# Optimization experiments

Hardware: AMD Instinct MI355X
Metric: run time of the kernel (lower is better)

## Reference

```python
import jax, jax.numpy as jnp
import numpy as np


def c2p_gather(feat, ind):
    # feat: [B, C, M] cell features; ind: [B, N, 2] (slot 0 = cell index)
    B, C, _ = feat.shape
    idx = ind[:, :, 0]                                   # [B, N]
    idx3 = jnp.broadcast_to(idx[:, None, :], (B, C, idx.shape[1]))
    return jnp.take_along_axis(feat, idx3, axis=2)       # [B, C, N]


def p2c_scatter(x, ind, num_cells):
    # x: [B, C, Nn] point features; ind: [B, Nn, 2]; scatter-add into [B, C, M]
    idx = ind[:, :, 0]                                   # [B, Nn]

    def per_batch(xb, ib):
        # xb: [C, Nn] -> segment_sum over points -> [M, C]
        return jax.ops.segment_sum(xb.T, ib, num_segments=num_cells).T

    return jax.vmap(per_batch)(x, idx)                   # [B, C, M]


def setup_inputs() -> dict:
    key = jax.random.key(0)
    ks = jax.random.split(key, 8)
    B, Cv, Cr, E, Co = 2, 64, 20, 64, 64
    Mv, Mr = 100000, 50000
    N = 262144            # gathered points; os=8 -> bundle=4 -> Nn=65536 nodes
    Nn = N // 4
    return {
        "v_feat": jax.random.normal(ks[0], (B, Cv, Mv), jnp.float32),
        "r_feat": jax.random.normal(ks[1], (B, Cr, Mr), jnp.float32),
        "Wq": jax.random.normal(ks[2], (E, Cr), jnp.float32) * 0.1,
        "Wk": jax.random.normal(ks[3], (E, Cv), jnp.float32) * 0.1,
        "Wv": jax.random.normal(ks[4], (E, Cv), jnp.float32) * 0.1,
        "Wo": jax.random.normal(ks[5], (Co, E), jnp.float32) * 0.1,
        "v2p_ind": jax.random.randint(ks[6], (B, N, 2), 0, Mv).astype(jnp.int64),
        "r2p_ind": jax.random.randint(ks[7], (B, Nn, 2), 0, Mr).astype(jnp.int64),
        "os": 8,
    }


def reference(v_feat, r_feat, Wq, Wk, Wv, Wo, v2p_ind, r2p_ind, os):
    bundle = max(1, int(os) // 2)
    B, Cv, _ = v_feat.shape
    Mr = r_feat.shape[2]

    # c2p gather of detached features (module calls .detach())
    v_pp = c2p_gather(jax.lax.stop_gradient(v_feat), v2p_ind)       # [B, Cv, N]
    N = v_pp.shape[2]
    Nn = N // bundle
    v_nodes = v_pp.reshape(B, Cv, Nn, bundle)                        # bundle splits
    r_pp = c2p_gather(jax.lax.stop_gradient(r_feat), r2p_ind)        # [B, Cr, Nn]

    # attent1d: query from r feature, keys/values from the neighbor bundle
    E = Wq.shape[0]
    q = jnp.einsum("ec,bcn->ben", Wq, r_pp)                          # [B, E, Nn]
    k = jnp.einsum("ec,bcnm->benm", Wk, v_nodes)                     # [B, E, Nn, bundle]
    v = jnp.einsum("ec,bcnm->benm", Wv, v_nodes)
    scores = jnp.einsum("ben,benm->bnm", q, k) / jnp.sqrt(jnp.float32(E))
    attn = jax.nn.softmax(scores, axis=-1)                           # over bundle
    agg = jnp.einsum("bnm,benm->ben", attn, v)                       # [B, E, Nn]
    xr = jnp.einsum("oe,ben->bon", Wo, agg)                          # [B, Co, Nn]

    # p2c scatter back to r-cell layout (size taken from r_feat)
    xr_mapped = p2c_scatter(xr, r2p_ind, Mr)                         # [B, Co, Mr]
    return xr_mapped
```

## Files before the change

### kernel.cpp

```cpp
#include <hip/hip_runtime.h>
#include <cstdint>

#define BB 2
#define CV 64
#define CR 20
#define EE 64
#define CO 64

__global__ __launch_bounds__(256) void k_prep(
    const float* __restrict__ Wq, const float* __restrict__ Wk,
    const float* __restrict__ Wv, const float* __restrict__ Wo,
    const int* __restrict__ r2p, float* __restrict__ G,
    float* __restrict__ H, int* __restrict__ flag) {
  int bid = blockIdx.x, t = threadIdx.x;
  if (bid < 5) {
    int idx = bid * 256 + t;
    if (idx < CR * CV) {
      int cr = idx / CV, cv = idx % CV;
      float s = 0.f;
      #pragma unroll
      for (int e = 0; e < EE; ++e) s += Wq[e * CR + cr] * Wk[e * CV + cv];
      G[idx] = s;
    }
  } else if (bid < 21) {
    int idx = (bid - 5) * 256 + t;
    int o = idx >> 6, c = idx & 63;
    float s = 0.f;
    #pragma unroll
    for (int e = 0; e < EE; ++e) s += Wo[o * EE + e] * Wv[e * CV + c];
    H[idx] = s;
  } else {
    __shared__ int any;
    if (t == 0) any = 0;
    __syncthreads();
    int nz = 0;
    for (int i = t; i < 4096; i += 256) nz |= r2p[2 * i + 1];
    if (nz) atomicOr(&any, 1);
    __syncthreads();
    if (t == 0) *flag = (any == 0) ? 4 : 2;
  }
}

__global__ __launch_bounds__(256) void k_transpose_v(
    const float* __restrict__ vf, float* __restrict__ vt, int Mv, int ntm) {
  __shared__ float tile[64][65];
  int b = blockIdx.x / ntm, tm = blockIdx.x % ntm;
  int m0 = tm * 64;
  int t = threadIdx.x;
  const float* src = vf + (size_t)b * CV * Mv;
  bool fast = ((Mv & 3) == 0) && (m0 + 64 <= Mv);
  if (fast) {
    #pragma unroll
    for (int k = 0; k < 4; ++k) {
      int c = k * 16 + (t >> 4), l16 = t & 15;
      float4 v = *(const float4*)&src[(size_t)c * Mv + m0 + 4 * l16];
      tile[c][4 * l16 + 0] = v.x;
      tile[c][4 * l16 + 1] = v.y;
      tile[c][4 * l16 + 2] = v.z;
      tile[c][4 * l16 + 3] = v.w;
    }
  } else {
    #pragma unroll
    for (int k = 0; k < 16; ++k) {
      int idx = t + k * 256;
      int c = idx >> 6, ml = idx & 63;
      int m = m0 + ml;
      tile[c][ml] = (m < Mv) ? src[(size_t)c * Mv + m] : 0.f;
    }
  }
  __syncthreads();
  float* dst = vt + (size_t)b * Mv * 64;
  if (fast) {
    #pragma unroll
    for (int k = 0; k < 4; ++k) {
      int ml = k * 16 + (t >> 4), l16 = t & 15;
      float4 w;
      w.x = tile[4 * l16 + 0][ml];
      w.y = tile[4 * l16 + 1][ml];
      w.z = tile[4 * l16 + 2][ml];
      w.w = tile[4 * l16 + 3][ml];
      *(float4*)&dst[(size_t)(m0 + ml) * 64 + 4 * l16] = w;
    }
  } else {
    #pragma unroll
    for (int k = 0; k < 16; ++k) {
      int idx = t + k * 256;
      int ml = idx >> 6, c = idx & 63;
      int m = m0 + ml;
      if (m < Mv) dst[(size_t)m * 64 + c] = tile[c][ml];
    }
  }
}

__global__ __launch_bounds__(256) void k_gq(
    const float* __restrict__ rf, const float* __restrict__ G,
    float* __restrict__ gq, int Mr, int ntj) {
  __shared__ float Gl[CR * 64];
  __shared__ float rt[CR][68];
  int b = blockIdx.x / ntj, tj = blockIdx.x % ntj;
  int j0 = tj * 64;
  int t = threadIdx.x;
  for (int idx = t; idx < CR * 64; idx += 256) Gl[idx] = G[idx];
  const float* src = rf + (size_t)b * CR * Mr;
  for (int idx = t; idx < CR * 64; idx += 256) {
    int c = idx >> 6, jl = idx & 63;
    int j = j0 + jl;
    rt[c][jl] = (j < Mr) ? src[(size_t)c * Mr + j] : 0.f;
  }
  __syncthreads();
  int ti = t & 15, tjq = t >> 4;
  float acc[4][4];
  #pragma unroll
  for (int a = 0; a < 4; ++a)
    #pragma unroll
    for (int q = 0; q < 4; ++q) acc[a][q] = 0.f;
  for (int c = 0; c < CR; ++c) {
    float4 gx = *(const float4*)&Gl[c * 64 + 4 * ti];
    float4 xj = *(const float4*)&rt[c][4 * tjq];
    #pragma unroll
    for (int a = 0; a < 4; ++a) {
      float xv = (a == 0) ? xj.x : (a == 1) ? xj.y : (a == 2) ? xj.z : xj.w;
      acc[a][0] += xv * gx.x;
      acc[a][1] += xv * gx.y;
      acc[a][2] += xv * gx.z;
      acc[a][3] += xv * gx.w;
    }
  }
  #pragma unroll
  for (int a = 0; a < 4; ++a) {
    int j = j0 + 4 * tjq + a;
    if (j < Mr) {
      float4 w = make_float4(acc[a][0], acc[a][1], acc[a][2], acc[a][3]);
      *(float4*)&gq[((size_t)b * Mr + j) * 64 + 4 * ti] = w;
    }
  }
}

template <int WS>
__device__ __forceinline__ void main_loop(
    const float* __restrict__ vt, const float* __restrict__ gq,
    const int* __restrict__ v2p, const int* __restrict__ r2p,
    float* __restrict__ xs, int Mv, int Mr, int N, int Nn, int P,
    int gw, int totWaves) {
  int stride = totWaves * 2;
  int base = gw * 2;
  if (base >= P) return;
  int b = (base >= Nn) ? 1 : 0;
  int n0 = base - b * Nn;
  int j0 = r2p[((size_t)b * Nn + n0) * WS];
  int j1 = r2p[((size_t)b * Nn + n0 + 1) * WS];
  const int* vi = v2p + ((size_t)b * N + (size_t)n0 * 4) * WS;
  int i00 = vi[0 * WS], i01 = vi[1 * WS], i02 = vi[2 * WS], i03 = vi[3 * WS];
  int i10 = vi[4 * WS], i11 = vi[5 * WS], i12 = vi[6 * WS], i13 = vi[7 * WS];
  int lane = threadIdx.x & 63;
  while (base < P) {
    const float* gqb = gq + (size_t)b * Mr * 64;
    const float* vb = vt + (size_t)b * Mv * 64;
    float q0 = gqb[(size_t)j0 * 64 + lane];
    float q1 = gqb[(size_t)j1 * 64 + lane];
    float c00 = vb[(size_t)i00 * 64 + lane];
    float c01 = vb[(size_t)i01 * 64 + lane];
    float c02 = vb[(size_t)i02 * 64 + lane];
    float c03 = vb[(size_t)i03 * 64 + lane];
    float c10 = vb[(size_t)i10 * 64 + lane];
    float c11 = vb[(size_t)i11 * 64 + lane];
    float c12 = vb[(size_t)i12 * 64 + lane];
    float c13 = vb[(size_t)i13 * 64 + lane];
    size_t sj0 = ((size_t)b * Mr + j0) * 64 + lane;
    size_t sj1 = ((size_t)b * Mr + j1) * 64 + lane;
    int nb = base + stride;
    int b2 = 0, pj0 = 0, pj1 = 0;
    int p00 = 0, p01 = 0, p02 = 0, p03 = 0, p10 = 0, p11 = 0, p12 = 0, p13 = 0;
    if (nb < P) {
      b2 = (nb >= Nn) ? 1 : 0;
      int n2 = nb - b2 * Nn;
      pj0 = r2p[((size_t)b2 * Nn + n2) * WS];
      pj1 = r2p[((size_t)b2 * Nn + n2 + 1) * WS];
      const int* vi2 = v2p + ((size_t)b2 * N + (size_t)n2 * 4) * WS;
      p00 = vi2[0 * WS]; p01 = vi2[1 * WS]; p02 = vi2[2 * WS]; p03 = vi2[3 * WS];
      p10 = vi2[4 * WS]; p11 = vi2[5 * WS]; p12 = vi2[6 * WS]; p13 = vi2[7 * WS];
    }
    float s00 = q0 * c00, s01 = q0 * c01, s02 = q0 * c02, s03 = q0 * c03;
    float s10 = q1 * c10, s11 = q1 * c11, s12 = q1 * c12, s13 = q1 * c13;
    #pragma unroll
    for (int off = 32; off > 0; off >>= 1) {
      s00 += __shfl_xor(s00, off); s01 += __shfl_xor(s01, off);
      s02 += __shfl_xor(s02, off); s03 += __shfl_xor(s03, off);
      s10 += __shfl_xor(s10, off); s11 += __shfl_xor(s11, off);
      s12 += __shfl_xor(s12, off); s13 += __shfl_xor(s13, off);
    }
    {
      float a = s00 * 0.125f, b3 = s01 * 0.125f, c3 = s02 * 0.125f, d = s03 * 0.125f;
      float mx = fmaxf(fmaxf(a, b3), fmaxf(c3, d));
      float e0 = __expf(a - mx), e1 = __expf(b3 - mx);
      float e2 = __expf(c3 - mx), e3 = __expf(d - mx);
      float inv = 1.f / (e0 + e1 + e2 + e3);
      float ag = (e0 * c00 + e1 * c01 + e2 * c02 + e3 * c03) * inv;
      atomicAdd(&xs[sj0], ag);
    }
    {
      float a = s10 * 0.125f, b3 = s11 * 0.125f, c3 = s12 * 0.125f, d = s13 * 0.125f;
      float mx = fmaxf(fmaxf(a, b3), fmaxf(c3, d));
      float e0 = __expf(a - mx), e1 = __expf(b3 - mx);
      float e2 = __expf(c3 - mx), e3 = __expf(d - mx);
      float inv = 1.f / (e0 + e1 + e2 + e3);
      float ag = (e0 * c10 + e1 * c11 + e2 * c12 + e3 * c13) * inv;
      atomicAdd(&xs[sj1], ag);
    }
    base = nb; b = b2; j0 = pj0; j1 = pj1;
    i00 = p00; i01 = p01; i02 = p02; i03 = p03;
    i10 = p10; i11 = p11; i12 = p12; i13 = p13;
  }
}

__global__ __launch_bounds__(256) void k_main(
    const float* __restrict__ vt, const float* __restrict__ gq,
    const int* __restrict__ v2p, const int* __restrict__ r2p,
    float* __restrict__ xs, const int* __restrict__ flag,
    int Mv, int Mr, int N, int Nn, int P, int totWaves) {
  int t = threadIdx.x;
  int gw = blockIdx.x * 4 + (t >> 6);
  if (*flag == 2)
    main_loop<2>(vt, gq, v2p, r2p, xs, Mv, Mr, N, Nn, P, gw, totWaves);
  else
    main_loop<4>(vt, gq, v2p, r2p, xs, Mv, Mr, N, Nn, P, gw, totWaves);
}

__device__ __forceinline__ int hsw(int fidx) {
  return fidx ^ (((fidx >> 8) & 7) << 2);
}

__global__ __launch_bounds__(256) void k_out_t(
    const float* __restrict__ xs, const float* __restrict__ H,
    float* __restrict__ out, int Mr, int ntj) {
  __shared__ float Hl[CO * CV];
  __shared__ float xt[64][68];
  int b = blockIdx.x / ntj, tj = blockIdx.x % ntj;
  int j0 = tj * 64;
  int t = threadIdx.x;
  for (int idx = t; idx < CO * CV; idx += 256) Hl[hsw(idx)] = H[idx];
  const float* src = xs + (size_t)b * Mr * 64;
  #pragma unroll
  for (int k = 0; k < 4; ++k) {
    int jl = k * 16 + (t >> 4), c4 = t & 15;
    int j = j0 + jl;
    float4 v = (j < Mr) ? *(const float4*)&src[(size_t)j * 64 + 4 * c4]
                        : make_float4(0.f, 0.f, 0.f, 0.f);
    *(float4*)&xt[jl][4 * c4] = v;
  }
  __syncthreads();
  int ti = t & 15;
  int tjq4 = t >> 4;
  float acc[4][4];
  #pragma unroll
  for (int a = 0; a < 4; ++a)
    #pragma unroll
    for (int q = 0; q < 4; ++q) acc[a][q] = 0.f;
  #pragma unroll 4
  for (int cq = 0; cq < 16; ++cq) {
    float4 xv[4], hb[4];
    #pragma unroll
    for (int a = 0; a < 4; ++a)
      xv[a] = *(const float4*)&xt[4 * tjq4 + a][4 * cq];
    #pragma unroll
    for (int q = 0; q < 4; ++q) {
      int row = 4 * ti + q;
      hb[q] = *(const float4*)&Hl[hsw(row * 64 + 4 * cq)];
    }
    #pragma unroll
    for (int a = 0; a < 4; ++a)
      #pragma unroll
      for (int q = 0; q < 4; ++q)
        acc[a][q] += xv[a].x * hb[q].x + xv[a].y * hb[q].y +
                     xv[a].z * hb[q].z + xv[a].w * hb[q].w;
  }
  __syncthreads();
  #pragma unroll
  for (int a = 0; a < 4; ++a)
    #pragma unroll
    for (int q = 0; q < 4; ++q)
      xt[4 * ti + q][4 * tjq4 + a] = acc[a][q];
  __syncthreads();
  float* dst = out + (size_t)b * CO * Mr;
  #pragma unroll
  for (int k = 0; k < 4; ++k) {
    int o = k * 16 + (t >> 4), j4 = t & 15;
    int j = j0 + 4 * j4;
    if (j + 3 < Mr) {
      *(float4*)&dst[(size_t)o * Mr + j] = *(const float4*)&xt[o][4 * j4];
    } else {
      #pragma unroll
      for (int i = 0; i < 4; ++i)
        if (j + i < Mr) dst[(size_t)o * Mr + j + i] = xt[o][4 * j4 + i];
    }
  }
}

extern "C" void kernel_launch(void* const* d_in, const int* in_sizes, int n_in,
                              void* d_out, int out_size, void* d_ws, size_t ws_size,
                              hipStream_t stream) {
  const float* v_feat = (const float*)d_in[0];
  const float* r_feat = (const float*)d_in[1];
  const float* Wq = (const float*)d_in[2];
  const float* Wk = (const float*)d_in[3];
  const float* Wv = (const float*)d_in[4];
  const float* Wo = (const float*)d_in[5];
  const int* v2p = (const int*)d_in[6];
  const int* r2p = (const int*)d_in[7];

  int Mv = in_sizes[0] / (BB * CV);
  int Mr = in_sizes[1] / (BB * CR);
  int N  = in_sizes[6] / (BB * 2);
  int Nn = in_sizes[7] / (BB * 2);

  float* ws = (float*)d_ws;
  float* vt = ws;
  float* gq = vt + (size_t)BB * Mv * 64;
  float* xs = gq + (size_t)BB * Mr * 64;
  float* G  = xs + (size_t)BB * Mr * 64;
  float* H  = G + CR * CV;
  int* flag = (int*)(H + CO * CV);
  float* out = (float*)d_out;

  hipMemsetAsync(xs, 0, (size_t)BB * Mr * 64 * sizeof(float), stream);

  k_prep<<<22, 256, 0, stream>>>(Wq, Wk, Wv, Wo, r2p, G, H, flag);

  int ntm = (Mv + 63) / 64;
  k_transpose_v<<<BB * ntm, 256, 0, stream>>>(v_feat, vt, Mv, ntm);

  int ntj = (Mr + 63) / 64;
  k_gq<<<BB * ntj, 256, 0, stream>>>(r_feat, G, gq, Mr, ntj);

  int P = BB * Nn;
  int blocks = 2048;
  k_main<<<blocks, 256, 0, stream>>>(vt, gq, v2p, r2p, xs, flag,
                                     Mv, Mr, N, Nn, P, blocks * 4);

  k_out_t<<<BB * ntj, 256, 0, stream>>>(xs, H, out, Mr, ntj);
}
```

Measured before the change: 220.8 us.

## Fuse setup kernels and remap main loop to 16 lanes per node with float4

Merges the memset, weight-prep and v-feature transpose into a single setup kernel to cut launch overhead. The main attention loop now gives each 16-lane group one node and loads float4 channel slices, so a wave handles four nodes per iteration with 16-lane shuffle reductions instead of full 64-lane ones. Index loads for the two-word layout use vector int4 reads. Each lane now issues four scalar atomics per node instead of one, and register pressure goes up.

```diff
diff --git a/kernel.cpp b/kernel.cpp
--- a/kernel.cpp
+++ b/kernel.cpp
@@ -6,15 +6,68 @@
 #define CR 20
 #define EE 64
 #define CO 64
-
-__global__ __launch_bounds__(256) void k_prep(
-    const float* __restrict__ Wq, const float* __restrict__ Wk,
-    const float* __restrict__ Wv, const float* __restrict__ Wo,
-    const int* __restrict__ r2p, float* __restrict__ G,
-    float* __restrict__ H, int* __restrict__ flag) {
+#define NZ 256
+
+__global__ __launch_bounds__(256) void k_setup(
+    const float* __restrict__ vf, const float* __restrict__ Wq,
+    const float* __restrict__ Wk, const float* __restrict__ Wv,
+    const float* __restrict__ Wo, const int* __restrict__ r2p,
+    float* __restrict__ vt, float* __restrict__ G, float* __restrict__ H,
+    int* __restrict__ flag, float4* __restrict__ xs4,
+    int Mv, int ntm, int NT, int xsE4) {
   int bid = blockIdx.x, t = threadIdx.x;
-  if (bid < 5) {
-    int idx = bid * 256 + t;
+  if (bid < NT) {
+    __shared__ float tile[64][65];
+    int b = bid / ntm, tm = bid % ntm;
+    int m0 = tm * 64;
+    const float* src = vf + (size_t)b * CV * Mv;
+    bool fast = ((Mv & 3) == 0) && (m0 + 64 <= Mv);
+    if (fast) {
+      #pragma unroll
+      for (int k = 0; k < 4; ++k) {
+        int c = k * 16 + (t >> 4), l16 = t & 15;
+        float4 v = *(const float4*)&src[(size_t)c * Mv + m0 + 4 * l16];
+        tile[c][4 * l16 + 0] = v.x;
+        tile[c][4 * l16 + 1] = v.y;
+        tile[c][4 * l16 + 2] = v.z;
+        tile[c][4 * l16 + 3] = v.w;
+      }
+    } else {
+      #pragma unroll
+      for (int k = 0; k < 16; ++k) {
+        int idx = t + k * 256;
+        int c = idx >> 6, ml = idx & 63;
+        int m = m0 + ml;
+        tile[c][ml] = (m < Mv) ? src[(size_t)c * Mv + m] : 0.f;
+      }
+    }
+    __syncthreads();
+    float* dst = vt + (size_t)b * Mv * 64;
+    if (fast) {
+      #pragma unroll
+      for (int k = 0; k < 4; ++k) {
+        int ml = k * 16 + (t >> 4), l16 = t & 15;
+        float4 w;
+        w.x = tile[4 * l16 + 0][ml];
+        w.y = tile[4 * l16 + 1][ml];
+        w.z = tile[4 * l16 + 2][ml];
+        w.w = tile[4 * l16 + 3][ml];
+        *(float4*)&dst[(size_t)(m0 + ml) * 64 + 4 * l16] = w;
+      }
+    } else {
+      #pragma unroll
+      for (int k = 0; k < 16; ++k) {
+        int idx = t + k * 256;
+        int ml = idx >> 6, c = idx & 63;
+        int m = m0 + ml;
+        if (m < Mv) dst[(size_t)m * 64 + c] = tile[c][ml];
+      }
+    }
+    return;
+  }
+  int r = bid - NT;
+  if (r < 5) {
+    int idx = r * 256 + t;
     if (idx < CR * CV) {
       int cr = idx / CV, cv = idx % CV;
       float s = 0.f;
@@ -22,14 +75,14 @@
       for (int e = 0; e < EE; ++e) s += Wq[e * CR + cr] * Wk[e * CV + cv];
       G[idx] = s;
     }
-  } else if (bid < 21) {
-    int idx = (bid - 5) * 256 + t;
+  } else if (r < 21) {
+    int idx = (r - 5) * 256 + t;
     int o = idx >> 6, c = idx & 63;
     float s = 0.f;
     #pragma unroll
     for (int e = 0; e < EE; ++e) s += Wo[o * EE + e] * Wv[e * CV + c];
     H[idx] = s;
-  } else {
+  } else if (r == 21) {
     __shared__ int any;
     if (t == 0) any = 0;
     __syncthreads();
@@ -38,57 +91,10 @@
     if (nz) atomicOr(&any, 1);
     __syncthreads();
     if (t == 0) *flag = (any == 0) ? 4 : 2;
-  }
-}
-
-__global__ __launch_bounds__(256) void k_transpose_v(
-    const float* __restrict__ vf, float* __restrict__ vt, int Mv, int ntm) {
-  __shared__ float tile[64][65];
-  int b = blockIdx.x / ntm, tm = blockIdx.x % ntm;
-  int m0 = tm * 64;
-  int t = threadIdx.x;
-  const float* src = vf + (size_t)b * CV * Mv;
-  bool fast = ((Mv & 3) == 0) && (m0 + 64 <= Mv);
-  if (fast) {
-    #pragma unroll
-    for (int k = 0; k < 4; ++k) {
-      int c = k * 16 + (t >> 4), l16 = t & 15;
-      float4 v = *(const float4*)&src[(size_t)c * Mv + m0 + 4 * l16];
-      tile[c][4 * l16 + 0] = v.x;
-      tile[c][4 * l16 + 1] = v.y;
-      tile[c][4 * l16 + 2] = v.z;
-      tile[c][4 * l16 + 3] = v.w;
-    }
   } else {
-    #pragma unroll
-    for (int k = 0; k < 16; ++k) {
-      int idx = t + k * 256;
-      int c = idx >> 6, ml = idx & 63;
-      int m = m0 + ml;
-      tile[c][ml] = (m < Mv) ? src[(size_t)c * Mv + m] : 0.f;
-    }
-  }
-  __syncthreads();
-  float* dst = vt + (size_t)b * Mv * 64;
-  if (fast) {
-    #pragma unroll
-    for (int k = 0; k < 4; ++k) {
-      int ml = k * 16 + (t >> 4), l16 = t & 15;
-      float4 w;
-      w.x = tile[4 * l16 + 0][ml];
-      w.y = tile[4 * l16 + 1][ml];
-      w.z = tile[4 * l16 + 2][ml];
-      w.w = tile[4 * l16 + 3][ml];
-      *(float4*)&dst[(size_t)(m0 + ml) * 64 + 4 * l16] = w;
-    }
-  } else {
-    #pragma unroll
-    for (int k = 0; k < 16; ++k) {
-      int idx = t + k * 256;
-      int ml = idx >> 6, c = idx & 63;
-      int m = m0 + ml;
-      if (m < Mv) dst[(size_t)m * 64 + c] = tile[c][ml];
-    }
+    int z = r - 22;
+    float4 zz = make_float4(0.f, 0.f, 0.f, 0.f);
+    for (int i = z * 256 + t; i < xsE4; i += NZ * 256) xs4[i] = zz;
   }
 }
 
@@ -137,79 +143,83 @@
 }
 
 template <int WS>
+__device__ __forceinline__ void load_idx(
+    const int* __restrict__ r2p, const int* __restrict__ v2p,
+    int p, int Nn, int N, int P,
+    int& b, int& j, int& i0, int& i1, int& i2, int& i3) {
+  if (p >= P) { b = 0; j = 0; i0 = i1 = i2 = i3 = 0; return; }
+  b = (p >= Nn) ? 1 : 0;
+  int n = p - b * Nn;
+  j = r2p[((size_t)b * Nn + n) * WS];
+  const int* vi = v2p + ((size_t)b * N + (size_t)n * 4) * WS;
+  if (WS == 2) {
+    int4 w0 = *(const int4*)vi;
+    int4 w1 = *(const int4*)(vi + 4);
+    i0 = w0.x; i1 = w0.z; i2 = w1.x; i3 = w1.z;
+  } else {
+    i0 = vi[0]; i1 = vi[1 * WS]; i2 = vi[2 * WS]; i3 = vi[3 * WS];
+  }
+}
+
+__device__ __forceinline__ float gred16(float h) {
+  h += __shfl_xor(h, 1);
+  h += __shfl_xor(h, 2);
+  h += __shfl_xor(h, 4);
+  h += __shfl_xor(h, 8);
+  return h;
+}
+
+template <int WS>
 __device__ __forceinline__ void main_loop(
     const float* __restrict__ vt, const float* __restrict__ gq,
     const int* __restrict__ v2p, const int* __restrict__ r2p,
     float* __restrict__ xs, int Mv, int Mr, int N, int Nn, int P,
     int gw, int totWaves) {
-  int stride = totWaves * 2;
-  int base = gw * 2;
+  int t = threadIdx.x;
+  int sl = t & 15, grp = (t >> 4) & 3;
+  int stride = totWaves * 4;
+  int base = gw * 4;
   if (base >= P) return;
-  int b = (base >= Nn) ? 1 : 0;
-  int n0 = base - b * Nn;
-  int j0 = r2p[((size_t)b * Nn + n0) * WS];
-  int j1 = r2p[((size_t)b * Nn + n0 + 1) * WS];
-  const int* vi = v2p + ((size_t)b * N + (size_t)n0 * 4) * WS;
-  int i00 = vi[0 * WS], i01 = vi[1 * WS], i02 = vi[2 * WS], i03 = vi[3 * WS];
-  int i10 = vi[4 * WS], i11 = vi[5 * WS], i12 = vi[6 * WS], i13 = vi[7 * WS];
-  int lane = threadIdx.x & 63;
-  while (base < P) {
+  int b, j, i0, i1, i2, i3;
+  load_idx<WS>(r2p, v2p, base + grp, Nn, N, P, b, j, i0, i1, i2, i3);
+  while (true) {
     const float* gqb = gq + (size_t)b * Mr * 64;
-    const float* vb = vt + (size_t)b * Mv * 64;
-    float q0 = gqb[(size_t)j0 * 64 + lane];
-    float q1 = gqb[(size_t)j1 * 64 + lane];
-    float c00 = vb[(size_t)i00 * 64 + lane];
-    float c01 = vb[(size_t)i01 * 64 + lane];
-    float c02 = vb[(size_t)i02 * 64 + lane];
-    float c03 = vb[(size_t)i03 * 64 + lane];
-    float c10 = vb[(size_t)i10 * 64 + lane];
-    float c11 = vb[(size_t)i11 * 64 + lane];
-    float c12 = vb[(size_t)i12 * 64 + lane];
-    float c13 = vb[(size_t)i13 * 64 + lane];
-    size_t sj0 = ((size_t)b * Mr + j0) * 64 + lane;
-    size_t sj1 = ((size_t)b * Mr + j1) * 64 + lane;
+    const float* vb  = vt + (size_t)b * Mv * 64;
+    float4 q4 = *(const float4*)&gqb[(size_t)j  * 64 + 4 * sl];
+    float4 c0 = *(const float4*)&vb [(size_t)i0 * 64 + 4 * sl];
+    float4 c1 = *(const float4*)&vb [(size_t)i1 * 64 + 4 * sl];
+    float4 c2 = *(const float4*)&vb [(size_t)i2 * 64 + 4 * sl];
+    float4 c3 = *(const float4*)&vb [(size_t)i3 * 64 + 4 * sl];
+    size_t sj = ((size_t)b * Mr + j) * 64 + 4 * sl;
+    bool vld = (base + grp) < P;
     int nb = base + stride;
-    int b2 = 0, pj0 = 0, pj1 = 0;
-    int p00 = 0, p01 = 0, p02 = 0, p03 = 0, p10 = 0, p11 = 0, p12 = 0, p13 = 0;
-    if (nb < P) {
-      b2 = (nb >= Nn) ? 1 : 0;
-      int n2 = nb - b2 * Nn;
-      pj0 = r2p[((size_t)b2 * Nn + n2) * WS];
-      pj1 = r2p[((size_t)b2 * Nn + n2 + 1) * WS];
-      const int* vi2 = v2p + ((size_t)b2 * N + (size_t)n2 * 4) * WS;
-      p00 = vi2[0 * WS]; p01 = vi2[1 * WS]; p02 = vi2[2 * WS]; p03 = vi2[3 * WS];
-      p10 = vi2[4 * WS]; p11 = vi2[5 * WS]; p12 = vi2[6 * WS]; p13 = vi2[7 * WS];
-    }
-    float s00 = q0 * c00, s01 = q0 * c01, s02 = q0 * c02, s03 = q0 * c03;
-    float s10 = q1 * c10, s11 = q1 * c11, s12 = q1 * c12, s13 = q1 * c13;
-    #pragma unroll
-    for (int off = 32; off > 0; off >>= 1) {
-      s00 += __shfl_xor(s00, off); s01 += __shfl_xor(s01, off);
-      s02 += __shfl_xor(s02, off); s03 += __shfl_xor(s03, off);
-      s10 += __shfl_xor(s10, off); s11 += __shfl_xor(s11, off);
-      s12 += __shfl_xor(s12, off); s13 += __shfl_xor(s13, off);
-    }
-    {
-      float a = s00 * 0.125f, b3 = s01 * 0.125f, c3 = s02 * 0.125f, d = s03 * 0.125f;
-      float mx = fmaxf(fmaxf(a, b3), fmaxf(c3, d));
-      float e0 = __expf(a - mx), e1 = __expf(b3 - mx);
-      float e2 = __expf(c3 - mx), e3 = __expf(d - mx);
-      float inv = 1.f / (e0 + e1 + e2 + e3);
-      float ag = (e0 * c00 + e1 * c01 + e2 * c02 + e3 * c03) * inv;
-      atomicAdd(&xs[sj0], ag);
-    }
-    {
-      float a = s10 * 0.125f, b3 = s11 * 0.125f, c3 = s12 * 0.125f, d = s13 * 0.125f;
-      float mx = fmaxf(fmaxf(a, b3), fmaxf(c3, d));
-      float e0 = __expf(a - mx), e1 = __expf(b3 - mx);
-      float e2 = __expf(c3 - mx), e3 = __expf(d - mx);
-      float inv = 1.f / (e0 + e1 + e2 + e3);
-      float ag = (e0 * c10 + e1 * c11 + e2 * c12 + e3 * c13) * inv;
-      atomicAdd(&xs[sj1], ag);
-    }
-    base = nb; b = b2; j0 = pj0; j1 = pj1;
-    i00 = p00; i01 = p01; i02 = p02; i03 = p03;
-    i10 = p10; i11 = p11; i12 = p12; i13 = p13;
+    int b2 = 0, j2 = 0, p0 = 0, p1 = 0, p2 = 0, p3 = 0;
+    bool more = nb < P;
+    if (more)
+      load_idx<WS>(r2p, v2p, nb + grp, Nn, N, P, b2, j2, p0, p1, p2, p3);
+    float s0 = gred16(q4.x * c0.x + q4.y * c0.y + q4.z * c0.z + q4.w * c0.w);
+    float s1 = gred16(q4.x * c1.x + q4.y * c1.y + q4.z * c1.z + q4.w * c1.w);
+    float s2 = gred16(q4.x * c2.x + q4.y * c2.y + q4.z * c2.z + q4.w * c2.w);
+    float s3 = gred16(q4.x * c3.x + q4.y * c3.y + q4.z * c3.z + q4.w * c3.w);
+    s0 *= 0.125f; s1 *= 0.125f; s2 *= 0.125f; s3 *= 0.125f;
+    float mx = fmaxf(fmaxf(s0, s1), fmaxf(s2, s3));
+    float e0 = __expf(s0 - mx), e1 = __expf(s1 - mx);
+    float e2 = __expf(s2 - mx), e3 = __expf(s3 - mx);
+    float inv = 1.f / (e0 + e1 + e2 + e3);
+    e0 *= inv; e1 *= inv; e2 *= inv; e3 *= inv;
+    float4 ag;
+    ag.x = e0 * c0.x + e1 * c1.x + e2 * c2.x + e3 * c3.x;
+    ag.y = e0 * c0.y + e1 * c1.y + e2 * c2.y + e3 * c3.y;
+    ag.z = e0 * c0.z + e1 * c1.z + e2 * c2.z + e3 * c3.z;
+    ag.w = e0 * c0.w + e1 * c1.w + e2 * c2.w + e3 * c3.w;
+    if (vld) {
+      atomicAdd(&xs[sj + 0], ag.x);
+      atomicAdd(&xs[sj + 1], ag.y);
+      atomicAdd(&xs[sj + 2], ag.z);
+      atomicAdd(&xs[sj + 3], ag.w);
+    }
+    if (!more) break;
+    base = nb; b = b2; j = j2; i0 = p0; i1 = p1; i2 = p2; i3 = p3;
   }
 }
 
@@ -218,8 +228,7 @@
     const int* __restrict__ v2p, const int* __restrict__ r2p,
     float* __restrict__ xs, const int* __restrict__ flag,
     int Mv, int Mr, int N, int Nn, int P, int totWaves) {
-  int t = threadIdx.x;
-  int gw = blockIdx.x * 4 + (t >> 6);
+  int gw = blockIdx.x * 4 + (threadIdx.x >> 6);
   if (*flag == 2)
     main_loop<2>(vt, gq, v2p, r2p, xs, Mv, Mr, N, Nn, P, gw, totWaves);
   else
@@ -322,12 +331,12 @@
   int* flag = (int*)(H + CO * CV);
   float* out = (float*)d_out;
 
-  hipMemsetAsync(xs, 0, (size_t)BB * Mr * 64 * sizeof(float), stream);
-
-  k_prep<<<22, 256, 0, stream>>>(Wq, Wk, Wv, Wo, r2p, G, H, flag);
-
   int ntm = (Mv + 63) / 64;
-  k_transpose_v<<<BB * ntm, 256, 0, stream>>>(v_feat, vt, Mv, ntm);
+  int NT = BB * ntm;
+  int xsE4 = (BB * Mr * 64) / 4;
+  k_setup<<<NT + 22 + NZ, 256, 0, stream>>>(v_feat, Wq, Wk, Wv, Wo, r2p,
+                                            vt, G, H, flag, (float4*)xs,
+                                            Mv, ntm, NT, xsE4);
 
   int ntj = (Mr + 63) / 64;
   k_gq<<<BB * ntj, 256, 0, stream>>>(r_feat, G, gq, Mr, ntj);
```

New measurement: 291.6 us. 32.0% more time.
